# Kernel tuning notes

Hardware: AMD Instinct MI355X
Metric: run time of the kernel (lower is better)

The kernel has to match this reference:

```python
import jax, jax.numpy as jnp
import numpy as np
import math

B, N, K, H = 2, 2048, 1024, 16
S = K // H  # head dim = 64


def apply_rope(t):
    # t: [b, h, N, s] -> rotary position embedding (rotate-half convention)
    s = t.shape[-1]
    pos = jnp.arange(t.shape[2], dtype=jnp.float32)
    inv_freq = 1.0 / (10000.0 ** (jnp.arange(0, s, 2, dtype=jnp.float32) / s))
    ang = pos[:, None] * inv_freq[None, :]               # [N, s/2]
    cos = jnp.concatenate([jnp.cos(ang), jnp.cos(ang)], axis=-1)  # [N, s]
    sin = jnp.concatenate([jnp.sin(ang), jnp.sin(ang)], axis=-1)
    t1, t2 = t[..., : s // 2], t[..., s // 2:]
    rot = jnp.concatenate([-t2, t1], axis=-1)
    return t * cos + rot * sin


def setup_inputs() -> dict:
    key = jax.random.key(0)
    ks = jax.random.split(key, 6)
    sc = 1.0 / math.sqrt(K)
    x = jax.random.normal(ks[0], (B, N, K), dtype=jnp.float32)
    Wq = jax.random.normal(ks[1], (K, K), dtype=jnp.float32) * sc
    Wk = jax.random.normal(ks[2], (K, K), dtype=jnp.float32) * sc
    Wv = jax.random.normal(ks[3], (K, K), dtype=jnp.float32) * sc
    Wu = jax.random.normal(ks[4], (K, K), dtype=jnp.float32) * sc
    bu = jax.random.normal(ks[5], (K,), dtype=jnp.float32) * 0.01
    mask = jnp.tril(jnp.ones((N, N), dtype=jnp.int32))  # causal
    return {"x": x, "Wq": Wq, "Wk": Wk, "Wv": Wv, "Wu": Wu, "bu": bu, "mask": mask}


def reference(x, Wq, Wk, Wv, Wu, bu, mask):
    b, n, k = x.shape
    h, s = H, S
    # torch Linear: y = x @ W.T
    def proj(W):
        return (x @ W.T).reshape(b, n, h, s).transpose(0, 2, 1, 3)  # [b,h,n,s]
    Q = apply_rope(proj(Wq))
    Kh = apply_rope(proj(Wk))
    V = proj(Wv)
    scores = jnp.einsum('bhqs,bhks->bhqk', Q, Kh) / math.sqrt(s)
    scores = jnp.where(mask[None, None, :, :] == 0, -jnp.inf, scores)
    attn = jax.nn.softmax(scores, axis=-1)
    out = jnp.einsum('bhqk,bhks->bhqs', attn, V)           # [b,h,n,s]
    out = out.transpose(0, 2, 1, 3).reshape(b, n, k)
    return out @ Wu.T + bu
```

## Files before the change

### kernel.cpp

```cpp
#include <hip/hip_runtime.h>
#include <hip/hip_bf16.h>

#define Bq 2
#define Nq 2048
#define Kq 1024
#define Hq 16
#define Sq 64
#define Mq (Bq * Nq)

typedef __attribute__((ext_vector_type(4))) float f32x4;
typedef __attribute__((ext_vector_type(8))) short bf16x8;

__device__ unsigned short g_xb[(size_t)Mq * Kq];
__device__ unsigned short g_Wqb[Kq * Kq];
__device__ unsigned short g_Wkb[Kq * Kq];
__device__ unsigned short g_Wvb[Kq * Kq];
__device__ unsigned short g_Wub[Kq * Kq];
__device__ unsigned short g_Qb[(size_t)Bq * Hq * Nq * Sq];
__device__ unsigned short g_Kb[(size_t)Bq * Hq * Nq * Sq];
__device__ unsigned short g_Vt[(size_t)Bq * Hq * Sq * Nq];
__device__ unsigned short g_Ao[(size_t)Mq * Kq];
__device__ __align__(16) float g_On[(size_t)32 * 16 * 3 * 128 * 64];
__device__ float g_Ol[32 * 16 * 3 * 128];

__constant__ signed char c_qt[30] = {15,15,15,14,14,14,13,13,13,12,12,12,11,11,10,10,9,9,8,8,7,7,6,6,5,4,3,2,1,0};
__constant__ signed char c_t0[30] = {0,11,22,0,10,20,0,10,19,0,9,18,0,12,0,11,0,10,0,9,0,8,0,7,0,0,0,0,0,0};
__constant__ signed char c_t1[30] = {11,22,32,10,20,30,10,19,28,9,18,26,12,24,11,22,10,20,9,18,8,16,7,14,12,10,8,6,4,2};
__constant__ signed char c_sp[30] = {0,1,2,0,1,2,0,1,2,0,1,2,0,1,0,1,0,1,0,1,0,1,0,1,0,0,0,0,0,0};
__constant__ signed char c_ns[30] = {3,3,3,3,3,3,3,3,3,3,3,3,2,2,2,2,2,2,2,2,2,2,2,2,1,1,1,1,1,1};

__device__ __forceinline__ unsigned short f2bf(float f) {
    union { float f; unsigned int i; } u; u.f = f;
    unsigned int r = u.i + 0x7FFF + ((u.i >> 16) & 1);
    return (unsigned short)(r >> 16);
}
__device__ __forceinline__ float bf2f(unsigned short u) {
    union { unsigned int i; float f; } v; v.i = ((unsigned int)u) << 16;
    return v.f;
}
__device__ __forceinline__ void async16(const unsigned short* g, unsigned short* l) {
    __builtin_amdgcn_global_load_lds(
        (const __attribute__((address_space(1))) void*)g,
        (__attribute__((address_space(3))) void*)l, 16, 0, 0);
}

__global__ __launch_bounds__(256) void convert_all_kernel(
    const float* __restrict__ x,  const float* __restrict__ wq,
    const float* __restrict__ wk, const float* __restrict__ wv,
    const float* __restrict__ wu)
{
    int i = blockIdx.x * 256 + threadIdx.x;
    const float* src; unsigned short* dst; int off;
    if (i < 1048576) { src = x; dst = g_xb; off = i; }
    else {
        int j = i - 1048576;
        int which = j >> 18;
        off = j & 262143;
        src = (which == 0) ? wq : (which == 1) ? wk : (which == 2) ? wv : wu;
        dst = (which == 0) ? g_Wqb : (which == 1) ? g_Wkb : (which == 2) ? g_Wvb : g_Wub;
    }
    float4 v = ((const float4*)src)[off];
    ushort4 o;
    o.x = f2bf(v.x); o.y = f2bf(v.y); o.z = f2bf(v.z); o.w = f2bf(v.w);
    ((ushort4*)dst)[off] = o;
}

__global__ __launch_bounds__(512, 2) void qkv_gemm_kernel()
{
    __shared__ __align__(16) unsigned short SLDS[65536];
    auto As = (unsigned short (*)[256][64])(SLDS);
    auto Bs = (unsigned short (*)[256][64])(SLDS + 32768);

    const int n0 = blockIdx.x * 256;
    const int m0 = blockIdx.y * 256;
    const int which = n0 >> 10;
    const unsigned short* A  = g_xb;
    const unsigned short* Bm = (which == 0) ? g_Wqb : (which == 1) ? g_Wkb : g_Wvb;
    const int nb = n0 & 1023;

    const int tid = threadIdx.x;
    const int w = tid >> 6, l = tid & 63;
    const int lane16 = l & 15, quad = l >> 4;
    const int wr = w >> 2, wc = w & 3;
    const int sr8 = l >> 3;
    const int sc  = ((l & 7) ^ sr8) * 8;
    const int rsw = lane16 & 7;

    f32x4 acc[8][4];
#pragma unroll
    for (int mf = 0; mf < 8; ++mf)
#pragma unroll
        for (int nf = 0; nf < 4; ++nf) acc[mf][nf] = (f32x4){0.f, 0.f, 0.f, 0.f};

#define STG_A(t, b, c) async16(A  + (size_t)(m0 + (c)*64 + w*8 + sr8) * Kq + (t)*64 + sc, \
                               &As[(b)][(c)*64 + w*8][0])
#define STG_B(t, b, c) async16(Bm + (size_t)(nb + (c)*64 + w*8 + sr8) * Kq + (t)*64 + sc, \
                               &Bs[(b)][(c)*64 + w*8][0])

    STG_B(0, 0, 0); STG_B(0, 0, 1); STG_B(0, 0, 2); STG_B(0, 0, 3);
    STG_A(0, 0, 0); STG_A(0, 0, 2); STG_A(0, 0, 1); STG_A(0, 0, 3);
    asm volatile("s_waitcnt vmcnt(2)" ::: "memory");
    __builtin_amdgcn_s_barrier();

    int cur = 0;
    for (int t = 0; t < 16; ++t) {
        const bool stg = (t + 1 < 16);
        const int nxt = cur ^ 1;
        bf16x8 bf[4][2];
#pragma unroll
        for (int q = 0; q < 4; ++q) {
            asm volatile("" ::: "memory");
            bf16x8 af[2][2];
            if (q == 0) {
#pragma unroll
                for (int nf = 0; nf < 4; ++nf)
#pragma unroll
                    for (int ks = 0; ks < 2; ++ks)
                        bf[nf][ks] = *(const bf16x8*)
                            &Bs[cur][wc * 64 + nf * 16 + lane16][((ks * 4 + quad) ^ rsw) * 8];
            }
#pragma unroll
            for (int m2 = 0; m2 < 2; ++m2)
#pragma unroll
                for (int ks = 0; ks < 2; ++ks)
                    af[m2][ks] = *(const bf16x8*)
                        &As[cur][wr * 128 + (q * 2 + m2) * 16 + lane16][((ks * 4 + quad) ^ rsw) * 8];
            if (stg) {
                if (q == 0) { STG_B(t + 1, nxt, 0); STG_B(t + 1, nxt, 1); }
                if (q == 1) { STG_B(t + 1, nxt, 2); STG_B(t + 1, nxt, 3); }
                if (q == 2) { STG_A(t + 1, nxt, 0); STG_A(t + 1, nxt, 2); }
                if (q == 3) { STG_A(t + 1, nxt, 1); STG_A(t + 1, nxt, 3); }
            }
            asm volatile("" ::: "memory");
            __builtin_amdgcn_s_barrier();
            asm volatile("s_waitcnt lgkmcnt(0)" ::: "memory");
            __builtin_amdgcn_sched_barrier(0);
            __builtin_amdgcn_s_setprio(1);
#pragma unroll
            for (int m2 = 0; m2 < 2; ++m2)
#pragma unroll
                for (int nf = 0; nf < 4; ++nf)
#pragma unroll
                    for (int ks = 0; ks < 2; ++ks)
                        acc[q * 2 + m2][nf] = __builtin_amdgcn_mfma_f32_16x16x32_bf16(
                            af[m2][ks], bf[nf][ks], acc[q * 2 + m2][nf], 0, 0, 0);
            __builtin_amdgcn_s_setprio(0);
            if (q == 1) {
                if (stg) asm volatile("s_waitcnt vmcnt(4)" ::: "memory");
                else     asm volatile("s_waitcnt vmcnt(0)" ::: "memory");
            }
            if (q == 3) {
                if (stg) asm volatile("s_waitcnt vmcnt(2)" ::: "memory");
                else     asm volatile("s_waitcnt vmcnt(0)" ::: "memory");
            }
            __builtin_amdgcn_s_barrier();
        }
        cur ^= 1;
    }
#undef STG_A
#undef STG_B

    const int h0q = nb >> 6;
    if (which < 2) {
        unsigned short* dst = (which == 0) ? g_Qb : g_Kb;
        const int h = h0q + wc;
        const float invf0 = exp2f((float)lane16 * -0.41524101f);
        const float invf1 = exp2f((float)(lane16 + 16) * -0.41524101f);
#pragma unroll
        for (int mf = 0; mf < 8; ++mf)
#pragma unroll
            for (int r = 0; r < 4; ++r) {
                int m = m0 + wr * 128 + mf * 16 + quad * 4 + r;
                int b = m >> 11, nn = m & 2047;
                float np = (float)nn;
                float a0 = np * invf0, a1 = np * invf1;
                float s0 = __sinf(a0), c0 = __cosf(a0);
                float s1 = __sinf(a1), c1 = __cosf(a1);
                float t10 = acc[mf][0][r], t20 = acc[mf][2][r];
                float t11 = acc[mf][1][r], t21 = acc[mf][3][r];
                unsigned short* dr = dst + (((size_t)b * Hq + h) * Nq + nn) * Sq + lane16;
                dr[0]  = f2bf(t10 * c0 - t20 * s0);
                dr[16] = f2bf(t11 * c1 - t21 * s1);
                dr[32] = f2bf(t20 * c0 + t10 * s0);
                dr[48] = f2bf(t21 * c1 + t11 * s1);
            }
    } else {
        unsigned short* T = SLDS;
        const int b = m0 >> 11, mcol = m0 & 2047;
#pragma unroll
        for (int pass = 0; pass < 2; ++pass) {
            __syncthreads();
            if (wr == pass) {
#pragma unroll
                for (int mf = 0; mf < 8; ++mf)
#pragma unroll
                    for (int nf = 0; nf < 4; ++nf)
#pragma unroll
                        for (int r = 0; r < 4; ++r)
                            T[(wc * 64 + nf * 16 + lane16) * 136 + mf * 16 + quad * 4 + r] =
                                f2bf(acc[mf][nf][r]);
            }
            __syncthreads();
            {
                int row = tid >> 1;
                int h = h0q + (row >> 6), s = row & 63;
                unsigned short* drow = g_Vt + (((size_t)b * Hq + h) * Sq + s) * Nq
                                        + mcol + pass * 128 + (tid & 1) * 64;
                const unsigned short* srow = T + row * 136 + (tid & 1) * 64;
#pragma unroll
                for (int jj = 0; jj < 8; ++jj)
                    *(uint4*)(drow + jj * 8) = *(const uint4*)(srow + jj * 8);
            }
        }
    }
}

__global__ __launch_bounds__(512) void attn_kernel()
{
    const int bh = blockIdx.x;
    const int y  = blockIdx.y;
    const int qt  = c_qt[y];
    const int t0  = c_t0[y];
    const int t1  = c_t1[y];
    const int sp  = c_sp[y];
    const int nsp = c_ns[y];
    const int q0 = qt * 128;
    const unsigned short* Qp = g_Qb + (size_t)bh * Nq * Sq;
    const unsigned short* Kp = g_Kb + (size_t)bh * Nq * Sq;
    const unsigned short* Vp = g_Vt + (size_t)bh * Sq * Nq;

    __shared__ __align__(16) unsigned short Ks[3][64][64];
    __shared__ __align__(16) unsigned short Vs[3][64][64];
    __shared__ __align__(16) unsigned short Ps[128][64];
    unsigned short* psf = &Ps[0][0];

    const int tid = threadIdx.x;
    const int w = tid >> 6, l = tid & 63;
    const int lane16 = l & 15, quad = l >> 4;
    const int sr = l >> 3;
    const int sc = ((l & 7) ^ sr) * 8;
    const int rsw = (lane16 & 7);

    bf16x8 be;
    {
        short o = (lane16 == 0) ? (short)0x3F80 : (short)0;
#pragma unroll
        for (int i = 0; i < 8; ++i) be[i] = o;
    }

    const int qlo = q0 + 16 * w;
    bf16x8 aq0 = *(const bf16x8*)(Qp + (size_t)(qlo + lane16) * Sq + quad * 8);
    bf16x8 aq1 = *(const bf16x8*)(Qp + (size_t)(qlo + lane16) * Sq + quad * 8 + 32);
    asm volatile("" : "+v"(aq0), "+v"(aq1));

    f32x4 Oacc[4];
    f32x4 Oext = (f32x4){0.f, 0.f, 0.f, 0.f};
#pragma unroll
    for (int ds = 0; ds < 4; ++ds) Oacc[ds] = (f32x4){0.f, 0.f, 0.f, 0.f};

    const float C1 = 0.18033688f;
    const float C2 = 11.54156036f;

#define STAGE(t, b)                                                           \
    do {                                                                      \
        int kn_ = (t) * 64;                                                   \
        async16(Kp + (size_t)(kn_ + 8 * w + sr) * Sq + sc, &Ks[(b)][8 * w][0]);\
        async16(Vp + (size_t)(8 * w + sr) * Nq + kn_ + sc, &Vs[(b)][8 * w][0]);\
    } while (0)

    STAGE(t0, 0);
    STAGE(t0 + 1, 1);
    asm volatile("s_waitcnt vmcnt(2)" ::: "memory");
    __builtin_amdgcn_s_barrier();
    __builtin_amdgcn_sched_barrier(0);

    int cur = 0;
    for (int kb = t0; kb < t1; ++kb) {
        if (kb + 2 < t1) STAGE(kb + 2, (kb - t0 + 2) % 3);

        if (kb * 64 <= qlo + 15) {
            f32x4 S[4];
#pragma unroll
            for (int kc = 0; kc < 4; ++kc) S[kc] = (f32x4){0.f, 0.f, 0.f, 0.f};
#pragma unroll
            for (int kc = 0; kc < 4; ++kc) {
                const unsigned short* krow = &Ks[cur][kc * 16 + lane16][0];
                bf16x8 bk0 = *(const bf16x8*)&krow[(quad ^ rsw) * 8];
                bf16x8 bk1 = *(const bf16x8*)&krow[((4 + quad) ^ rsw) * 8];
                S[kc] = __builtin_amdgcn_mfma_f32_16x16x32_bf16(aq0, bk0, S[kc], 0, 0, 0);
                S[kc] = __builtin_amdgcn_mfma_f32_16x16x32_bf16(aq1, bk1, S[kc], 0, 0, 0);
            }

            const int qbase = qlo + quad * 4;
            if (kb * 64 + 63 > qlo) {
#pragma unroll
                for (int kc = 0; kc < 4; ++kc) {
                    int kpos = kb * 64 + kc * 16 + lane16;
#pragma unroll
                    for (int r = 0; r < 4; ++r)
                        S[kc][r] = (kpos <= qbase + r) ? exp2f(fmaf(S[kc][r], C1, -C2)) : 0.0f;
                }
            } else {
#pragma unroll
                for (int kc = 0; kc < 4; ++kc)
#pragma unroll
                    for (int r = 0; r < 4; ++r)
                        S[kc][r] = exp2f(fmaf(S[kc][r], C1, -C2));
            }

#pragma unroll
            for (int kc = 0; kc < 4; ++kc)
#pragma unroll
                for (int r = 0; r < 4; ++r) {
                    int prow = 16 * w + quad * 4 + r;
                    psf[(prow * 64 + kc * 16 + lane16) ^ ((prow & 7) << 3)] =
                        (unsigned short)(__float_as_uint(S[kc][r]) >> 16);
                }

            const int prow2 = 16 * w + lane16;
#pragma unroll
            for (int kk = 0; kk < 2; ++kk) {
                bf16x8 pa = *(const bf16x8*)(psf +
                    ((prow2 * 64 + kk * 32 + quad * 8) ^ (rsw << 3)));
#pragma unroll
                for (int ds = 0; ds < 4; ++ds) {
                    bf16x8 vb = *(const bf16x8*)&Vs[cur][ds * 16 + lane16][((kk * 4 + quad) ^ rsw) * 8];
                    Oacc[ds] = __builtin_amdgcn_mfma_f32_16x16x32_bf16(pa, vb, Oacc[ds], 0, 0, 0);
                }
                Oext = __builtin_amdgcn_mfma_f32_16x16x32_bf16(pa, be, Oext, 0, 0, 0);
            }
        }

        __builtin_amdgcn_sched_barrier(0);
        if (kb + 2 < t1) {
            asm volatile("s_waitcnt vmcnt(2)" ::: "memory");
        } else {
            asm volatile("s_waitcnt vmcnt(0)" ::: "memory");
        }
        __builtin_amdgcn_s_barrier();
        __builtin_amdgcn_sched_barrier(0);
        cur = (cur == 2) ? 0 : cur + 1;
    }
#undef STAGE

    if (nsp == 1) {
        const int b = bh >> 4, h = bh & 15;
        float inv[4];
#pragma unroll
        for (int r = 0; r < 4; ++r) {
            float lr = __shfl(Oext[r], quad * 16, 64);
            inv[r] = 1.0f / lr;
        }
#pragma unroll
        for (int ds = 0; ds < 4; ++ds)
#pragma unroll
            for (int r = 0; r < 4; ++r) {
                int nn = qlo + quad * 4 + r;
                g_Ao[((size_t)b * Nq + nn) * Kq + h * Sq + ds * 16 + lane16] =
                    f2bf(Oacc[ds][r] * inv[r]);
            }
    } else {
        float* On = g_On + (((size_t)bh * 16 + qt) * 3 + sp) * (128 * 64);
        float* Ol = g_Ol + (((size_t)bh * 16 + qt) * 3 + sp) * 128;
#pragma unroll
        for (int r = 0; r < 4; ++r) {
            float lr = __shfl(Oext[r], quad * 16, 64);
            if (lane16 == 0) Ol[16 * w + quad * 4 + r] = lr;
        }
#pragma unroll
        for (int ds = 0; ds < 4; ++ds)
#pragma unroll
            for (int r = 0; r < 4; ++r)
                On[(16 * w + quad * 4 + r) * 64 + ds * 16 + lane16] = Oacc[ds][r];
    }
}

__global__ __launch_bounds__(256) void attn_combine_kernel()
{
    const int bh = blockIdx.x;
    const int qt = 6 + blockIdx.y;
    const int nsp = (qt >= 12) ? 3 : 2;
    const int tid = threadIdx.x;
    const int row = tid >> 1;
    const int ch  = (tid & 1) * 32;
    const size_t sb = ((size_t)bh * 16 + qt) * 3;
    const float* On0 = g_On + (sb + 0) * (128 * 64);
    const float* On1 = g_On + (sb + 1) * (128 * 64);
    const float* On2 = g_On + (sb + 2) * (128 * 64);
    const float* Ol  = g_Ol + sb * 128;

    float lsum = Ol[row] + Ol[128 + row];
    if (nsp == 3) lsum += Ol[256 + row];
    float inv = 1.0f / lsum;

    const int b = bh >> 4, h = bh & 15, nn = qt * 128 + row;
    unsigned short* dst = g_Ao + ((size_t)b * Nq + nn) * Kq + h * Sq + ch;

#pragma unroll
    for (int j = 0; j < 8; ++j) {
        int o = row * 64 + ch + j * 4;
        f32x4 v = *(const f32x4*)(On0 + o);
        v += *(const f32x4*)(On1 + o);
        if (nsp == 3) v += *(const f32x4*)(On2 + o);
        ushort4 u;
        u.x = f2bf(v[0] * inv); u.y = f2bf(v[1] * inv);
        u.z = f2bf(v[2] * inv); u.w = f2bf(v[3] * inv);
        ((ushort4*)dst)[j] = u;
    }
}

__global__ __launch_bounds__(512, 1) void out_gemm_kernel(
    const float* __restrict__ bu, float* __restrict__ out)
{
    __shared__ __align__(16) unsigned short SLDS[49152];
    auto As = (unsigned short (*)[256][64])(SLDS);
    auto Bs = (unsigned short (*)[128][64])(SLDS + 32768);

    const int n0 = blockIdx.x * 128;
    const int m0 = blockIdx.y * 256;

    const int tid = threadIdx.x;
    const int w = tid >> 6, l = tid & 63;
    const int lane16 = l & 15, quad = l >> 4;
    const int wr = w >> 2, wc = w & 3;
    const int sr8 = l >> 3;
    const int sc  = ((l & 7) ^ sr8) * 8;
    const int rsw = lane16 & 7;

    f32x4 acc[8][2];
#pragma unroll
    for (int mf = 0; mf < 8; ++mf)
#pragma unroll
        for (int nf = 0; nf < 2; ++nf) acc[mf][nf] = (f32x4){0.f, 0.f, 0.f, 0.f};

#define OST_A(t, b, c) async16(g_Ao  + (size_t)(m0 + (c)*64 + w*8 + sr8) * Kq + (t)*64 + sc, \
                               &As[(b)][(c)*64 + w*8][0])
#define OST_B(t, b, c) async16(g_Wub + (size_t)(n0 + (c)*64 + w*8 + sr8) * Kq + (t)*64 + sc, \
                               &Bs[(b)][(c)*64 + w*8][0])

    OST_B(0, 0, 0); OST_B(0, 0, 1);
    OST_A(0, 0, 0); OST_A(0, 0, 2);
    OST_A(0, 0, 1); OST_A(0, 0, 3);
    asm volatile("s_waitcnt vmcnt(2)" ::: "memory");
    __builtin_amdgcn_s_barrier();

    int cur = 0;
    for (int t = 0; t < 16; ++t) {
        const bool stg = (t + 1 < 16);
        const int nxt = cur ^ 1;
        bf16x8 bf[2][2];
#pragma unroll
        for (int q = 0; q < 4; ++q) {
            asm volatile("" ::: "memory");
            bf16x8 af[2][2];
            if (q == 0) {
#pragma unroll
                for (int nf = 0; nf < 2; ++nf)
#pragma unroll
                    for (int ks = 0; ks < 2; ++ks)
                        bf[nf][ks] = *(const bf16x8*)
                            &Bs[cur][wc * 32 + nf * 16 + lane16][((ks * 4 + quad) ^ rsw) * 8];
            }
#pragma unroll
            for (int m2 = 0; m2 < 2; ++m2)
#pragma unroll
                for (int ks = 0; ks < 2; ++ks)
                    af[m2][ks] = *(const bf16x8*)
                        &As[cur][wr * 128 + (q * 2 + m2) * 16 + lane16][((ks * 4 + quad) ^ rsw) * 8];
            if (stg) {
                if (q == 0) { OST_B(t + 1, nxt, 0); OST_B(t + 1, nxt, 1); }
                if (q == 1) { OST_A(t + 1, nxt, 0); OST_A(t + 1, nxt, 2); }
                if (q == 2) { OST_A(t + 1, nxt, 1); OST_A(t + 1, nxt, 3); }
            }
            asm volatile("" ::: "memory");
            __builtin_amdgcn_s_barrier();
            asm volatile("s_waitcnt lgkmcnt(0)" ::: "memory");
            __builtin_amdgcn_sched_barrier(0);
            __builtin_amdgcn_s_setprio(1);
#pragma unroll
            for (int m2 = 0; m2 < 2; ++m2)
#pragma unroll
                for (int nf = 0; nf < 2; ++nf)
#pragma unroll
                    for (int ks = 0; ks < 2; ++ks)
                        acc[q * 2 + m2][nf] = __builtin_amdgcn_mfma_f32_16x16x32_bf16(
                            af[m2][ks], bf[nf][ks], acc[q * 2 + m2][nf], 0, 0, 0);
            __builtin_amdgcn_s_setprio(0);
            if (q == 1) {
                if (stg) asm volatile("s_waitcnt vmcnt(4)" ::: "memory");
                else     asm volatile("s_waitcnt vmcnt(0)" ::: "memory");
            }
            if (q == 3) {
                if (stg) asm volatile("s_waitcnt vmcnt(2)" ::: "memory");
                else     asm volatile("s_waitcnt vmcnt(0)" ::: "memory");
            }
            __builtin_amdgcn_s_barrier();
        }
        cur ^= 1;
    }
#undef OST_A
#undef OST_B

#pragma unroll
    for (int mf = 0; mf < 8; ++mf)
#pragma unroll
        for (int nf = 0; nf < 2; ++nf)
#pragma unroll
            for (int r = 0; r < 4; ++r) {
                int m = m0 + wr * 128 + mf * 16 + quad * 4 + r;
                int n = n0 + wc * 32 + nf * 16 + lane16;
                out[(size_t)m * Kq + n] = acc[mf][nf][r] + bu[n];
            }
}

extern "C" void kernel_launch(void* const* d_in, const int* in_sizes, int n_in,
                              void* d_out, int out_size, void* d_ws, size_t ws_size,
                              hipStream_t stream)
{
    const float* x  = (const float*)d_in[0];
    const float* Wq = (const float*)d_in[1];
    const float* Wk = (const float*)d_in[2];
    const float* Wv = (const float*)d_in[3];
    const float* Wu = (const float*)d_in[4];
    const float* bu = (const float*)d_in[5];
    float* out = (float*)d_out;

    convert_all_kernel<<<8192, 256, 0, stream>>>(x, Wq, Wk, Wv, Wu);
    qkv_gemm_kernel<<<dim3(12, 16), 512, 0, stream>>>();
    attn_kernel<<<dim3(32, 30), 512, 0, stream>>>();
    attn_combine_kernel<<<dim3(32, 10), 256, 0, stream>>>();
    out_gemm_kernel<<<dim3(8, 16), 512, 0, stream>>>(bu, out);
}
```

Before: 214.6 us.

## Transpose QK^T MFMA and pass P via lane shuffles instead of LDS

Swaps MFMA operand order so the score tile comes out transposed (keys along rows per lane), then packs the bf16 probabilities with v_perm and redistributes them across lanes with __shfl to form the A operand of the PV MFMA. This removes the shared-memory P buffer and its write/read round trip, freeing LDS. It adds 16 cross-lane shuffles plus selects per tile, and the causal mask indexing changes to match the new layout.

After: 217.5 us. No clear change (+1.3%).

```diff
diff --git a/kernel.cpp b/kernel.cpp
--- a/kernel.cpp
+++ b/kernel.cpp
@@ -231,8 +231,6 @@
 
     __shared__ __align__(16) unsigned short Ks[3][64][64];
     __shared__ __align__(16) unsigned short Vs[3][64][64];
-    __shared__ __align__(16) unsigned short Ps[128][64];
-    unsigned short* psf = &Ps[0][0];
 
     const int tid = threadIdx.x;
     const int w = tid >> 6, l = tid & 63;
@@ -261,6 +259,10 @@
     const float C1 = 0.18033688f;
     const float C2 = 11.54156036f;
 
+    const int qpos = qlo + lane16;
+    const int srcA = 32 * (quad & 1) + lane16;
+    const int srcB = srcA + 16;
+
 #define STAGE(t, b)                                                           \
     do {                                                                      \
         int kn_ = (t) * 64;                                                   \
@@ -281,47 +283,59 @@
         if (kb * 64 <= qlo + 15) {
             f32x4 S[4];
 #pragma unroll
-            for (int kc = 0; kc < 4; ++kc) S[kc] = (f32x4){0.f, 0.f, 0.f, 0.f};
-#pragma unroll
-            for (int kc = 0; kc < 4; ++kc) {
-                const unsigned short* krow = &Ks[cur][kc * 16 + lane16][0];
-                bf16x8 bk0 = *(const bf16x8*)&krow[(quad ^ rsw) * 8];
-                bf16x8 bk1 = *(const bf16x8*)&krow[((4 + quad) ^ rsw) * 8];
-                S[kc] = __builtin_amdgcn_mfma_f32_16x16x32_bf16(aq0, bk0, S[kc], 0, 0, 0);
-                S[kc] = __builtin_amdgcn_mfma_f32_16x16x32_bf16(aq1, bk1, S[kc], 0, 0, 0);
-            }
-
-            const int qbase = qlo + quad * 4;
+            for (int kf = 0; kf < 4; ++kf) S[kf] = (f32x4){0.f, 0.f, 0.f, 0.f};
+#pragma unroll
+            for (int kf = 0; kf < 4; ++kf) {
+                const unsigned short* krow = &Ks[cur][kf * 16 + lane16][0];
+                bf16x8 ak0 = *(const bf16x8*)&krow[(quad ^ rsw) * 8];
+                bf16x8 ak1 = *(const bf16x8*)&krow[((4 + quad) ^ rsw) * 8];
+                S[kf] = __builtin_amdgcn_mfma_f32_16x16x32_bf16(ak0, aq0, S[kf], 0, 0, 0);
+                S[kf] = __builtin_amdgcn_mfma_f32_16x16x32_bf16(ak1, aq1, S[kf], 0, 0, 0);
+            }
+
             if (kb * 64 + 63 > qlo) {
 #pragma unroll
-                for (int kc = 0; kc < 4; ++kc) {
-                    int kpos = kb * 64 + kc * 16 + lane16;
-#pragma unroll
-                    for (int r = 0; r < 4; ++r)
-                        S[kc][r] = (kpos <= qbase + r) ? exp2f(fmaf(S[kc][r], C1, -C2)) : 0.0f;
+                for (int kf = 0; kf < 4; ++kf) {
+#pragma unroll
+                    for (int r = 0; r < 4; ++r) {
+                        int kpos = kb * 64 + kf * 16 + quad * 4 + r;
+                        S[kf][r] = (kpos <= qpos) ? exp2f(fmaf(S[kf][r], C1, -C2)) : 0.0f;
+                    }
                 }
             } else {
 #pragma unroll
-                for (int kc = 0; kc < 4; ++kc)
+                for (int kf = 0; kf < 4; ++kf)
 #pragma unroll
                     for (int r = 0; r < 4; ++r)
-                        S[kc][r] = exp2f(fmaf(S[kc][r], C1, -C2));
-            }
-
-#pragma unroll
-            for (int kc = 0; kc < 4; ++kc)
-#pragma unroll
-                for (int r = 0; r < 4; ++r) {
-                    int prow = 16 * w + quad * 4 + r;
-                    psf[(prow * 64 + kc * 16 + lane16) ^ ((prow & 7) << 3)] =
-                        (unsigned short)(__float_as_uint(S[kc][r]) >> 16);
+                        S[kf][r] = exp2f(fmaf(S[kf][r], C1, -C2));
+            }
+
+            unsigned int cvt[4][2];
+#pragma unroll
+            for (int c = 0; c < 4; ++c)
+#pragma unroll
+                for (int p = 0; p < 2; ++p)
+                    cvt[c][p] = __builtin_amdgcn_perm(
+                        __float_as_uint(S[c][2 * p + 1]),
+                        __float_as_uint(S[c][2 * p]), 0x07060302u);
+
+            unsigned int lo_[4][2], hi_[4][2];
+#pragma unroll
+            for (int c = 0; c < 4; ++c)
+#pragma unroll
+                for (int p = 0; p < 2; ++p) {
+                    lo_[c][p] = (unsigned int)__shfl((int)cvt[c][p], srcA, 64);
+                    hi_[c][p] = (unsigned int)__shfl((int)cvt[c][p], srcB, 64);
                 }
 
-            const int prow2 = 16 * w + lane16;
 #pragma unroll
             for (int kk = 0; kk < 2; ++kk) {
-                bf16x8 pa = *(const bf16x8*)(psf +
-                    ((prow2 * 64 + kk * 32 + quad * 8) ^ (rsw << 3)));
+                union { unsigned int u[4]; bf16x8 v; } pu;
+                pu.u[0] = (quad < 2) ? lo_[2 * kk][0] : lo_[2 * kk + 1][0];
+                pu.u[1] = (quad < 2) ? lo_[2 * kk][1] : lo_[2 * kk + 1][1];
+                pu.u[2] = (quad < 2) ? hi_[2 * kk][0] : hi_[2 * kk + 1][0];
+                pu.u[3] = (quad < 2) ? hi_[2 * kk][1] : hi_[2 * kk + 1][1];
+                bf16x8 pa = pu.v;
 #pragma unroll
                 for (int ds = 0; ds < 4; ++ds) {
                     bf16x8 vb = *(const bf16x8*)&Vs[cur][ds * 16 + lane16][((kk * 4 + quad) ^ rsw) * 8];
```

## Widen attention KV stage to 128 keys with double buffering

Applied to the files above, without the earlier changes.

Each attention pipeline stage now loads 128 keys (two 64-key halves of K and V) instead of 64, and uses double buffering instead of a three-deep ring. The per-block tile ranges and split tables are halved to match. This halves the number of waitcnt and barrier points per block and issues larger async batches. In exchange, shared memory per block grows, prefetch depth drops from two tiles ahead to one, and every iteration now waits for all outstanding loads.

Result: no change. 211.5 us (-1.5%).

```diff
diff --git a/kernel.cpp b/kernel.cpp
--- a/kernel.cpp
+++ b/kernel.cpp
@@ -24,8 +24,8 @@
 __device__ float g_Ol[32 * 16 * 3 * 128];
 
 __constant__ signed char c_qt[30] = {15,15,15,14,14,14,13,13,13,12,12,12,11,11,10,10,9,9,8,8,7,7,6,6,5,4,3,2,1,0};
-__constant__ signed char c_t0[30] = {0,11,22,0,10,20,0,10,19,0,9,18,0,12,0,11,0,10,0,9,0,8,0,7,0,0,0,0,0,0};
-__constant__ signed char c_t1[30] = {11,22,32,10,20,30,10,19,28,9,18,26,12,24,11,22,10,20,9,18,8,16,7,14,12,10,8,6,4,2};
+__constant__ signed char c_t0[30] = {0,6,11,0,5,10,0,5,10,0,5,9,0,6,0,6,0,5,0,5,0,4,0,4,0,0,0,0,0,0};
+__constant__ signed char c_t1[30] = {6,11,16,5,10,15,5,10,14,5,9,13,6,12,6,11,5,10,5,9,4,8,4,7,6,5,4,3,2,1};
 __constant__ signed char c_sp[30] = {0,1,2,0,1,2,0,1,2,0,1,2,0,1,0,1,0,1,0,1,0,1,0,1,0,0,0,0,0,0};
 __constant__ signed char c_ns[30] = {3,3,3,3,3,3,3,3,3,3,3,3,2,2,2,2,2,2,2,2,2,2,2,2,1,1,1,1,1,1};
 
@@ -229,8 +229,8 @@
     const unsigned short* Kp = g_Kb + (size_t)bh * Nq * Sq;
     const unsigned short* Vp = g_Vt + (size_t)bh * Sq * Nq;
 
-    __shared__ __align__(16) unsigned short Ks[3][64][64];
-    __shared__ __align__(16) unsigned short Vs[3][64][64];
+    __shared__ __align__(16) unsigned short Ks[2][2][64][64];
+    __shared__ __align__(16) unsigned short Vs[2][2][64][64];
     __shared__ __align__(16) unsigned short Ps[128][64];
     unsigned short* psf = &Ps[0][0];
 
@@ -261,85 +261,86 @@
     const float C1 = 0.18033688f;
     const float C2 = 11.54156036f;
 
-#define STAGE(t, b)                                                           \
-    do {                                                                      \
-        int kn_ = (t) * 64;                                                   \
-        async16(Kp + (size_t)(kn_ + 8 * w + sr) * Sq + sc, &Ks[(b)][8 * w][0]);\
-        async16(Vp + (size_t)(8 * w + sr) * Nq + kn_ + sc, &Vs[(b)][8 * w][0]);\
+#define STAGE(t, b)                                                              \
+    do {                                                                         \
+        int kn_ = (t) * 128;                                                     \
+        async16(Kp + (size_t)(kn_ + 8 * w + sr) * Sq + sc,      &Ks[(b)][0][8 * w][0]); \
+        async16(Kp + (size_t)(kn_ + 64 + 8 * w + sr) * Sq + sc, &Ks[(b)][1][8 * w][0]); \
+        async16(Vp + (size_t)(8 * w + sr) * Nq + kn_ + sc,      &Vs[(b)][0][8 * w][0]); \
+        async16(Vp + (size_t)(8 * w + sr) * Nq + kn_ + 64 + sc, &Vs[(b)][1][8 * w][0]); \
     } while (0)
 
     STAGE(t0, 0);
-    STAGE(t0 + 1, 1);
-    asm volatile("s_waitcnt vmcnt(2)" ::: "memory");
+    asm volatile("s_waitcnt vmcnt(0)" ::: "memory");
     __builtin_amdgcn_s_barrier();
     __builtin_amdgcn_sched_barrier(0);
 
     int cur = 0;
     for (int kb = t0; kb < t1; ++kb) {
-        if (kb + 2 < t1) STAGE(kb + 2, (kb - t0 + 2) % 3);
-
-        if (kb * 64 <= qlo + 15) {
-            f32x4 S[4];
-#pragma unroll
-            for (int kc = 0; kc < 4; ++kc) S[kc] = (f32x4){0.f, 0.f, 0.f, 0.f};
-#pragma unroll
-            for (int kc = 0; kc < 4; ++kc) {
-                const unsigned short* krow = &Ks[cur][kc * 16 + lane16][0];
-                bf16x8 bk0 = *(const bf16x8*)&krow[(quad ^ rsw) * 8];
-                bf16x8 bk1 = *(const bf16x8*)&krow[((4 + quad) ^ rsw) * 8];
-                S[kc] = __builtin_amdgcn_mfma_f32_16x16x32_bf16(aq0, bk0, S[kc], 0, 0, 0);
-                S[kc] = __builtin_amdgcn_mfma_f32_16x16x32_bf16(aq1, bk1, S[kc], 0, 0, 0);
-            }
-
-            const int qbase = qlo + quad * 4;
-            if (kb * 64 + 63 > qlo) {
+        if (kb + 1 < t1) STAGE(kb + 1, cur ^ 1);
+
+#pragma unroll
+        for (int hh = 0; hh < 2; ++hh) {
+            const int kbase = kb * 128 + hh * 64;
+            if (kbase <= qlo + 15) {
+                f32x4 S[4];
+#pragma unroll
+                for (int kc = 0; kc < 4; ++kc) S[kc] = (f32x4){0.f, 0.f, 0.f, 0.f};
 #pragma unroll
                 for (int kc = 0; kc < 4; ++kc) {
-                    int kpos = kb * 64 + kc * 16 + lane16;
-#pragma unroll
-                    for (int r = 0; r < 4; ++r)
-                        S[kc][r] = (kpos <= qbase + r) ? exp2f(fmaf(S[kc][r], C1, -C2)) : 0.0f;
+                    const unsigned short* krow = &Ks[cur][hh][kc * 16 + lane16][0];
+                    bf16x8 bk0 = *(const bf16x8*)&krow[(quad ^ rsw) * 8];
+                    bf16x8 bk1 = *(const bf16x8*)&krow[((4 + quad) ^ rsw) * 8];
+                    S[kc] = __builtin_amdgcn_mfma_f32_16x16x32_bf16(aq0, bk0, S[kc], 0, 0, 0);
+                    S[kc] = __builtin_amdgcn_mfma_f32_16x16x32_bf16(aq1, bk1, S[kc], 0, 0, 0);
                 }
-            } else {
+
+                const int qbase = qlo + quad * 4;
+                if (kbase + 63 > qlo) {
+#pragma unroll
+                    for (int kc = 0; kc < 4; ++kc) {
+                        int kpos = kbase + kc * 16 + lane16;
+#pragma unroll
+                        for (int r = 0; r < 4; ++r)
+                            S[kc][r] = (kpos <= qbase + r) ? exp2f(fmaf(S[kc][r], C1, -C2)) : 0.0f;
+                    }
+                } else {
+#pragma unroll
+                    for (int kc = 0; kc < 4; ++kc)
+#pragma unroll
+                        for (int r = 0; r < 4; ++r)
+                            S[kc][r] = exp2f(fmaf(S[kc][r], C1, -C2));
+                }
+
 #pragma unroll
                 for (int kc = 0; kc < 4; ++kc)
 #pragma unroll
-                    for (int r = 0; r < 4; ++r)
-                        S[kc][r] = exp2f(fmaf(S[kc][r], C1, -C2));
-            }
-
-#pragma unroll
-            for (int kc = 0; kc < 4; ++kc)
-#pragma unroll
-                for (int r = 0; r < 4; ++r) {
-                    int prow = 16 * w + quad * 4 + r;
-                    psf[(prow * 64 + kc * 16 + lane16) ^ ((prow & 7) << 3)] =
-                        (unsigned short)(__float_as_uint(S[kc][r]) >> 16);
+                    for (int r = 0; r < 4; ++r) {
+                        int prow = 16 * w + quad * 4 + r;
+                        psf[(prow * 64 + kc * 16 + lane16) ^ ((prow & 7) << 3)] =
+                            (unsigned short)(__float_as_uint(S[kc][r]) >> 16);
+                    }
+
+                const int prow2 = 16 * w + lane16;
+#pragma unroll
+                for (int kk = 0; kk < 2; ++kk) {
+                    bf16x8 pa = *(const bf16x8*)(psf +
+                        ((prow2 * 64 + kk * 32 + quad * 8) ^ (rsw << 3)));
+#pragma unroll
+                    for (int ds = 0; ds < 4; ++ds) {
+                        bf16x8 vb = *(const bf16x8*)&Vs[cur][hh][ds * 16 + lane16][((kk * 4 + quad) ^ rsw) * 8];
+                        Oacc[ds] = __builtin_amdgcn_mfma_f32_16x16x32_bf16(pa, vb, Oacc[ds], 0, 0, 0);
+                    }
+                    Oext = __builtin_amdgcn_mfma_f32_16x16x32_bf16(pa, be, Oext, 0, 0, 0);
                 }
-
-            const int prow2 = 16 * w + lane16;
-#pragma unroll
-            for (int kk = 0; kk < 2; ++kk) {
-                bf16x8 pa = *(const bf16x8*)(psf +
-                    ((prow2 * 64 + kk * 32 + quad * 8) ^ (rsw << 3)));
-#pragma unroll
-                for (int ds = 0; ds < 4; ++ds) {
-                    bf16x8 vb = *(const bf16x8*)&Vs[cur][ds * 16 + lane16][((kk * 4 + quad) ^ rsw) * 8];
-                    Oacc[ds] = __builtin_amdgcn_mfma_f32_16x16x32_bf16(pa, vb, Oacc[ds], 0, 0, 0);
-                }
-                Oext = __builtin_amdgcn_mfma_f32_16x16x32_bf16(pa, be, Oext, 0, 0, 0);
             }
         }
 
         __builtin_amdgcn_sched_barrier(0);
-        if (kb + 2 < t1) {
-            asm volatile("s_waitcnt vmcnt(2)" ::: "memory");
-        } else {
-            asm volatile("s_waitcnt vmcnt(0)" ::: "memory");
-        }
+        asm volatile("s_waitcnt vmcnt(0)" ::: "memory");
         __builtin_amdgcn_s_barrier();
         __builtin_amdgcn_sched_barrier(0);
-        cur = (cur == 2) ? 0 : cur + 1;
+        cur ^= 1;
     }
 #undef STAGE
 
```
